# Performance work log

Hardware: AMD Instinct MI355X
Metric: run time of the kernel (lower is better)

Reference implementation:

```python
import jax, jax.numpy as jnp
import numpy as np

BODY_EDGES = [(0, 2), (0, 5), (2, 7), (5, 8), (11, 12), (0, 11), (0, 12), (7, 11), (8, 12), (11, 13), (13, 15), (12, 14), (14, 16), (11, 23), (12, 24), (23, 24), (11, 24), (12, 23)]
N_JOINTS = 33
N_FEAT = 52
HIDDEN = 128
BN_EPS = 1e-5


def _make_adj():
    a = np.eye(N_JOINTS, dtype=np.float32)
    for i, j in BODY_EDGES:
        a[i, j] = 1.0
        a[j, i] = 1.0
    deg = np.clip(a.sum(1), 1.0, None)
    d = deg ** -0.5
    return jnp.asarray(d[:, None] * a * d[None, :])


def setup_inputs() -> dict:
    key = jax.random.key(0)
    ks = iter(jax.random.split(key, 40))
    B, T = 64, 256
    def lin(k, i, o):
        return jax.random.normal(k, (i, o), jnp.float32) / np.sqrt(i)
    inp = {
        'x': jax.random.normal(next(ks), (B, T, N_JOINTS, N_FEAT), jnp.float32),
        'adj': _make_adj(),
        # layer 0: in 52 -> out 128 (has skip linear)
        'W0': lin(next(ks), N_FEAT, HIDDEN), 'b0': jax.random.normal(next(ks), (HIDDEN,)) * 0.02,
        'S0': lin(next(ks), N_FEAT, HIDDEN), 'sb0': jax.random.normal(next(ks), (HIDDEN,)) * 0.02,
        'g0': 1.0 + 0.1 * jax.random.normal(next(ks), (HIDDEN,)), 'be0': 0.1 * jax.random.normal(next(ks), (HIDDEN,)),
        'm0': 0.1 * jax.random.normal(next(ks), (HIDDEN,)), 'v0': 1.0 + 0.1 * jax.random.uniform(next(ks), (HIDDEN,)),
        # layers 1,2: 128 -> 128 (identity skip)
        'W1': lin(next(ks), HIDDEN, HIDDEN), 'b1': jax.random.normal(next(ks), (HIDDEN,)) * 0.02,
        'g1': 1.0 + 0.1 * jax.random.normal(next(ks), (HIDDEN,)), 'be1': 0.1 * jax.random.normal(next(ks), (HIDDEN,)),
        'm1': 0.1 * jax.random.normal(next(ks), (HIDDEN,)), 'v1': 1.0 + 0.1 * jax.random.uniform(next(ks), (HIDDEN,)),
        'W2': lin(next(ks), HIDDEN, HIDDEN), 'b2': jax.random.normal(next(ks), (HIDDEN,)) * 0.02,
        'g2': 1.0 + 0.1 * jax.random.normal(next(ks), (HIDDEN,)), 'be2': 0.1 * jax.random.normal(next(ks), (HIDDEN,)),
        'm2': 0.1 * jax.random.normal(next(ks), (HIDDEN,)), 'v2': 1.0 + 0.1 * jax.random.uniform(next(ks), (HIDDEN,)),
        # temporal attention MLP: 128 -> 128 -> 1
        'tW1': lin(next(ks), HIDDEN, HIDDEN), 'tb1': jax.random.normal(next(ks), (HIDDEN,)) * 0.02,
        'tW2': lin(next(ks), HIDDEN, 1), 'tb2': jax.random.normal(next(ks), (1,)) * 0.02,
    }
    return inp


def _gcn(h, adj, W, b, g, be, m, v, skip):
    # adjacency mix: [B*T, J, D_in]
    a = jnp.einsum('nm,bmd->bnd', adj, h)
    z = a @ W + b
    z = (z - m) * jax.lax.rsqrt(v + BN_EPS) * g + be  # eval-mode BatchNorm1d
    return jax.nn.gelu(z, approximate=False) + skip


def reference(x, adj, W0, b0, S0, sb0, g0, be0, m0, v0,
              W1, b1, g1, be1, m1, v1,
              W2, b2, g2, be2, m2, v2,
              tW1, tb1, tW2, tb2):
    B, T, J, Fd = x.shape
    h = x.reshape(B * T, J, Fd)
    h = _gcn(h, adj, W0, b0, g0, be0, m0, v0, h @ S0 + sb0)
    h = _gcn(h, adj, W1, b1, g1, be1, m1, v1, h)
    h = _gcn(h, adj, W2, b2, g2, be2, m2, v2, h)
    # dropout inactive (eval mode)
    xt = h.mean(axis=1).reshape(B, T, -1)                  # [B, T, H]
    score = jax.nn.gelu(xt @ tW1 + tb1, approximate=False) @ tW2 + tb2  # [B, T, 1]
    attn = jax.nn.softmax(score, axis=1)
    return (xt * attn).sum(axis=1)                         # [B, H]
```

## Files before the change

kernel.cpp:

```cpp
#include <hip/hip_runtime.h>
#include <hip/hip_bf16.h>
#include <math.h>


#define NJ 33
#define NF 52
#define NH 128
#define NT 256
#define NB 64
#define NSAMP (NB*NT)
#define SPB 2
#define NBLKS (NSAMP/SPB)
#define HSTR 136
#define PSTR 40

typedef unsigned short u16;
typedef _Float16 f16;
typedef f16   half8 __attribute__((ext_vector_type(8)));
typedef f16   h2    __attribute__((ext_vector_type(2)));
typedef float f32x4 __attribute__((ext_vector_type(4)));

#define HO_W0    0
#define HO_S0    8192
#define HO_W1    16384
#define HO_W2    32768
#define HO_TW1   49152
#define HO_ADJ32 65536
#define H_TOTAL  66560
#define FO_BASE  (H_TOTAL/2)
#define FO_A0    (FO_BASE+0)
#define FO_SB0   (FO_BASE+768)
#define FO_TB1   (FO_BASE+896)
#define FO_TW2   (FO_BASE+1024)
#define FO_FLG   (FO_BASE+1152)
#define FO_XT    (FO_BASE+1280)
#define FO_SC    (FO_XT + NSAMP*NH)

__device__ __forceinline__ float bf2f(u16 u) { return __uint_as_float(((unsigned)u) << 16); }
__device__ __forceinline__ float ldv(const void* p, long i, int f) {
    float r;
    if (f) r = bf2f(((const u16*)p)[i]);
    else   r = ((const float*)p)[i];
    return r;
}
__device__ int detect_bf16(const void* p) {
    const u16* q = (const u16*)p;
    int nz = 0, ok = 0;
#pragma unroll
    for (int k = 0; k < 64; k++) {
        u16 u = q[k];
        if (u & 0x7FFF) {
            nz++;
            int e = (u >> 7) & 0xFF;
            ok += (e >= 0x40 && e <= 0xBF) ? 1 : 0;
        }
    }
    return (nz == 0) || (ok * 20 >= nz * 19);
}

__device__ __forceinline__ float gelu_c(float x) {
    float xc = fminf(fmaxf(x, -8.f), 8.f);
    float u  = xc * fmaf(xc * xc, 0.10294324f, 2.3022082f);
#if __has_builtin(__builtin_amdgcn_exp2f)
    float e  = __builtin_amdgcn_exp2f(u);
#else
    float e  = exp2f(u);
#endif
#if __has_builtin(__builtin_amdgcn_rcpf)
    float tt = (e - 1.f) * __builtin_amdgcn_rcpf(e + 1.f);
#else
    float tt = (e - 1.f) / (e + 1.f);
#endif
    float hx = 0.5f * x;
    return fmaf(hx, tt, hx);
}

#define MFMA16(a, b, c) __builtin_amdgcn_mfma_f32_16x16x32_f16(a, b, c, 0, 0, 0)

__global__ __launch_bounds__(256) void prep(
    const void* x, const void* adj,
    const void* W0, const void* b0, const void* S0, const void* sb0,
    const void* g0, const void* be0, const void* m0, const void* v0,
    const void* W1, const void* b1, const void* g1, const void* be1, const void* m1, const void* v1,
    const void* W2, const void* b2, const void* g2, const void* be2, const void* m2, const void* v2,
    const void* tW1, const void* tb1, const void* tW2,
    void* ws)
{
    f16* H = (f16*)ws; float* F = (float*)ws;
    const int bi = blockIdx.x, t = threadIdx.x;
    if (bi == 0) {
        const int fW = detect_bf16(W0), fS = detect_bf16(S0);
        for (int i = t; i < NF * 128; i += 256) {
            int k = i >> 7, n = i & 127;
            H[HO_W0 + n * 64 + k] = (f16)ldv(W0, i, fW);
            H[HO_S0 + n * 64 + k] = (f16)ldv(S0, i, fS);
        }
        for (int i = t; i < 128 * 16; i += 256) {
            int n = i >> 4, k = 48 + (i & 15);
            if (k >= NF) { H[HO_W0 + n * 64 + k] = (f16)0.f; H[HO_S0 + n * 64 + k] = (f16)0.f; }
        }
    } else if (bi == 1) {
        const int f = detect_bf16(W1);
        for (int i = t; i < 128 * 128; i += 256) {
            int k = i >> 7, n = i & 127;
            H[HO_W1 + n * 128 + k] = (f16)ldv(W1, i, f);
        }
    } else if (bi == 2) {
        if (t == 0) ((int*)F)[FO_FLG] = detect_bf16(x);
        const int f = detect_bf16(W2);
        for (int i = t; i < 128 * 128; i += 256) {
            int k = i >> 7, n = i & 127;
            H[HO_W2 + n * 128 + k] = (f16)ldv(W2, i, f);
        }
    } else if (bi == 3) {
        const int f = detect_bf16(tW1);
        for (int i = t; i < 128 * 128; i += 256) {
            int k = i >> 7, n = i & 127;
            H[HO_TW1 + n * 128 + k] = (f16)ldv(tW1, i, f);
        }
    } else {
        if (t < 128) {
            int c = t;
            {
                float g = ldv(g0,c,detect_bf16(g0)), be = ldv(be0,c,detect_bf16(be0));
                float m = ldv(m0,c,detect_bf16(m0)), v = ldv(v0,c,detect_bf16(v0));
                float b = ldv(b0,c,detect_bf16(b0));
                float A = g * rsqrtf(v + 1e-5f);
                F[FO_A0 + 0*256 + c] = A; F[FO_A0 + 0*256 + 128 + c] = (b - m)*A + be;
            }
            {
                float g = ldv(g1,c,detect_bf16(g1)), be = ldv(be1,c,detect_bf16(be1));
                float m = ldv(m1,c,detect_bf16(m1)), v = ldv(v1,c,detect_bf16(v1));
                float b = ldv(b1,c,detect_bf16(b1));
                float A = g * rsqrtf(v + 1e-5f);
                F[FO_A0 + 1*256 + c] = A; F[FO_A0 + 1*256 + 128 + c] = (b - m)*A + be;
            }
            {
                float g = ldv(g2,c,detect_bf16(g2)), be = ldv(be2,c,detect_bf16(be2));
                float m = ldv(m2,c,detect_bf16(m2)), v = ldv(v2,c,detect_bf16(v2));
                float b = ldv(b2,c,detect_bf16(b2));
                float A = g * rsqrtf(v + 1e-5f);
                F[FO_A0 + 2*256 + c] = A; F[FO_A0 + 2*256 + 128 + c] = (b - m)*A + be;
            }
            F[FO_SB0 + c] = ldv(sb0, c, detect_bf16(sb0));
            F[FO_TB1 + c] = ldv(tb1, c, detect_bf16(tb1));
            F[FO_TW2 + c] = ldv(tW2, c, detect_bf16(tW2));
        }
        const int fA = detect_bf16(adj);
        for (int i = t; i < 1024; i += 256) {
            int r = i >> 5, c = i & 31;
            float v = (r < 25 && c < 25) ? ldv(adj, (long)r*NJ + c, fA) : 0.f;
            H[HO_ADJ32 + i] = (f16)v;
        }
    }
}

#define PTWRITE(ACC)                                                            \
    _Pragma("unroll")                                                           \
    for (int mt = 0; mt < 4; mt++) {                                            \
        const int fF = mt >> 1;                                                 \
        const int jb = (mt & 1) * 16;                                           \
        _Pragma("unroll")                                                       \
        for (int nt = 0; nt < 2; nt++) {                                        \
            f16* pp = Pt + (fF*128 + (nt ? c1 : c0))*PSTR;                      \
            _Pragma("unroll")                                                   \
            for (int r2 = 0; r2 < 4; r2 += 2) {                                 \
                int j0 = jb + q*4 + r2;                                         \
                if (j0 + 1 < 25) {                                              \
                    h2 v2w = { (f16)ACC[mt][nt][r2], (f16)ACC[mt][nt][r2+1] };  \
                    *(h2*)(pp + j0) = v2w;                                      \
                } else if (j0 < 25) {                                           \
                    pp[j0] = (f16)ACC[mt][nt][r2];                              \
                }                                                               \
            }                                                                   \
        }                                                                       \
    }

#define ADJEPI(L, WRHB) {                                                       \
    f32x4 zac[2][2][2];                                                         \
    _Pragma("unroll")                                                           \
    for (int fF = 0; fF < 2; fF++) {                                            \
        _Pragma("unroll")                                                       \
        for (int nt = 0; nt < 2; nt++) {                                        \
            half8 bz = *(const half8*)(Pt + (fF*128 + (nt?c1:c0))*PSTR + q*8);  \
            zac[fF][0][nt] = MFMA16(afadj0, bz, z4);                            \
            zac[fF][1][nt] = MFMA16(afadj1, bz, z4);                            \
        }                                                                       \
    }                                                                           \
    _Pragma("unroll")                                                           \
    for (int nt = 0; nt < 2; nt++) {                                            \
        const int cc = nt ? c1 : c0;                                            \
        const float Av = rA[L][nt], Dv = rD[L][nt];                             \
        _Pragma("unroll")                                                       \
        for (int fF = 0; fF < 2; fF++) {                                        \
            _Pragma("unroll")                                                   \
            for (int m2 = 0; m2 < 2; m2++) {                                    \
                _Pragma("unroll")                                               \
                for (int r4 = 0; r4 < 4; r4++) {                                \
                    float zv = (m2 == 0) ? zac[fF][0][nt][r4]                   \
                             : (jlt[r4] ? zac[fF][1][nt][r4]                    \
                                        : acc[2*fF+1][nt][r4]);                 \
                    float hnew = gelu_c(fmaf(zv, Av, Dv)) + hz[fF][m2][nt][r4]; \
                    hz[fF][m2][nt][r4] = hnew;                                  \
                    if (WRHB)                                                   \
                        hb[((2*fF+m2)*16 + q*4 + r4)*HSTR + cc] = (f16)hnew;    \
                }                                                               \
            }                                                                   \
            {                                                                   \
                float hnew = gelu_c(fmaf(acc[4][nt][fF], Av, Dv)) + h32[fF][nt];\
                h32[fF][nt] = (q == 0) ? hnew : 0.f;                            \
                if (WRHB && q == 0)                                             \
                    hb[(64 + fF)*HSTR + cc] = (f16)hnew;                        \
            }                                                                   \
        }                                                                       \
    }                                                                           \
}

#define GEMM128(WOFF)                                                           \
    {                                                                           \
        half8 bf[2][4];                                                         \
        _Pragma("unroll")                                                       \
        for (int nt = 0; nt < 2; nt++)                                          \
            _Pragma("unroll")                                                   \
            for (int ks = 0; ks < 4; ks++)                                      \
                bf[nt][ks] = *(const half8*)(HW + (WOFF) + (nt?c1:c0)*128 + ks*32 + q*8); \
        _Pragma("unroll")                                                       \
        for (int mt = 0; mt < 5; mt++) { acc[mt][0] = z4; acc[mt][1] = z4; }    \
        _Pragma("unroll")                                                       \
        for (int mt = 0; mt < 5; mt++) {                                        \
            const int m = mt*16 + ml;                                           \
            _Pragma("unroll")                                                   \
            for (int ks = 0; ks < 4; ks++) {                                    \
                half8 af = *(const half8*)(hb + m*HSTR + ks*32 + q*8);          \
                acc[mt][0] = MFMA16(af, bf[0][ks], acc[mt][0]);                 \
                acc[mt][1] = MFMA16(af, bf[1][ks], acc[mt][1]);                 \
            }                                                                   \
        }                                                                       \
    }

#define GCN_BODY                                                                \
    const f16* HW = (const f16*)ws;                                             \
    float* F = (float*)ws;                                                      \
    float* xt_g = F + FO_XT;                                                    \
    float* sc_g = F + FO_SC;                                                    \
    const int t = threadIdx.x, lane = t & 63, wv = t >> 6;                      \
    const int q = lane >> 4, ml = lane & 15;                                    \
    const int n0 = wv * 32;                                                     \
    const int c0 = n0 + ml, c1 = n0 + 16 + ml;                                  \
    const f32x4 z4 = {0.f, 0.f, 0.f, 0.f};                                      \
    const bool jlt[4] = { q <= 2, q <= 1, q <= 1, q <= 1 };                     \
    const half8 zero8 = {(f16)0.f,(f16)0.f,(f16)0.f,(f16)0.f,(f16)0.f,(f16)0.f,(f16)0.f,(f16)0.f}; \
    _Pragma("unroll")                                                           \
    for (int i = t; i < 512; i += 256) {                                        \
        int fF = i >> 8, rem = i & 255, n = rem >> 1, chh = rem & 1;            \
        *(half8*)(Pt + (fF*128 + n)*PSTR + 24 + chh*8) = zero8;                 \
    }                                                                           \
    float rA[3][2], rD[3][2];                                                   \
    _Pragma("unroll")                                                           \
    for (int L = 0; L < 3; L++) {                                               \
        rA[L][0] = F[FO_A0 + L*256 + c0];        rA[L][1] = F[FO_A0 + L*256 + c1];       \
        rD[L][0] = F[FO_A0 + L*256 + 128 + c0];  rD[L][1] = F[FO_A0 + L*256 + 128 + c1]; \
    }                                                                           \
    const float sb0a = F[FO_SB0 + c0], sb0b = F[FO_SB0 + c1];                   \
    half8 afadj0 = *(const half8*)(HW + HO_ADJ32 + ml*32 + q*8);                \
    half8 afadj1 = *(const half8*)(HW + HO_ADJ32 + (16+ml)*32 + q*8);           \
    __syncthreads();                                                            \
    {                                                                           \
        const int fX = ((const int*)F)[FO_FLG];                                 \
        const long xb = (long)blockIdx.x * (SPB * NJ * NF);                     \
        _Pragma("unroll 1")                                                     \
        for (int it = 0; it < 3; it++) {                                        \
            int g = t + it * 256;                                               \
            if (g < 66 * 8) {                                                   \
                int r = g >> 3, blk = g & 7;                                    \
                int fF = (r >= 33) ? 1 : 0;                                     \
                int j = r - 33 * fF;                                            \
                int fr = (j < 32) ? (fF * 32 + j) : (64 + fF);                  \
                half8 o;                                                        \
                if (!fX) {                                                      \
                    const float* base = (const float*)x + xb + (long)r * NF + blk * 8; \
                    if (blk < 6) {                                              \
                        float4 v0 = *(const float4*)base;                       \
                        float4 v1 = *(const float4*)(base + 4);                 \
                        o[0]=(f16)v0.x; o[1]=(f16)v0.y; o[2]=(f16)v0.z; o[3]=(f16)v0.w; \
                        o[4]=(f16)v1.x; o[5]=(f16)v1.y; o[6]=(f16)v1.z; o[7]=(f16)v1.w; \
                    } else if (blk == 6) {                                      \
                        float4 v0 = *(const float4*)base;                       \
                        o = zero8;                                              \
                        o[0]=(f16)v0.x; o[1]=(f16)v0.y; o[2]=(f16)v0.z; o[3]=(f16)v0.w; \
                    } else o = zero8;                                           \
                } else {                                                        \
                    long rb = xb + (long)r * NF;                                \
                    _Pragma("unroll")                                           \
                    for (int i = 0; i < 8; i++) {                               \
                        int cx = blk * 8 + i;                                   \
                        o[i] = (f16)(cx < NF ? bf2f(((const u16*)x)[rb + cx]) : 0.f); \
                    }                                                           \
                }                                                               \
                *(half8*)(hb + fr * HSTR + blk * 8) = o;                        \
            }                                                                   \
        }                                                                       \
    }                                                                           \
    __syncthreads();                                                            \
    f32x4 acc[5][2];                                                            \
    float hz[2][2][2][4];                                                       \
    float h32[2][2];                                                            \
    {                                                                           \
        half8 bw[2][2], bs[2][2];                                               \
        _Pragma("unroll")                                                       \
        for (int nt = 0; nt < 2; nt++) {                                        \
            int n = nt ? c1 : c0;                                               \
            _Pragma("unroll")                                                   \
            for (int ks = 0; ks < 2; ks++) {                                    \
                bw[nt][ks] = *(const half8*)(HW + HO_W0 + n*64 + ks*32 + q*8);  \
                bs[nt][ks] = *(const half8*)(HW + HO_S0 + n*64 + ks*32 + q*8);  \
            }                                                                   \
        }                                                                       \
        f32x4 acs[5][2];                                                        \
        _Pragma("unroll")                                                       \
        for (int mt = 0; mt < 5; mt++) { acc[mt][0]=z4; acc[mt][1]=z4; acs[mt][0]=z4; acs[mt][1]=z4; } \
        _Pragma("unroll")                                                       \
        for (int mt = 0; mt < 5; mt++) {                                        \
            const int m = mt*16 + ml;                                           \
            half8 a0 = *(const half8*)(hb + m*HSTR + q*8);                      \
            half8 a1 = *(const half8*)(hb + m*HSTR + 32 + q*8);                 \
            acc[mt][0] = MFMA16(a0, bw[0][0], acc[mt][0]);                      \
            acc[mt][0] = MFMA16(a1, bw[0][1], acc[mt][0]);                      \
            acc[mt][1] = MFMA16(a0, bw[1][0], acc[mt][1]);                      \
            acc[mt][1] = MFMA16(a1, bw[1][1], acc[mt][1]);                      \
            acs[mt][0] = MFMA16(a0, bs[0][0], acs[mt][0]);                      \
            acs[mt][0] = MFMA16(a1, bs[0][1], acs[mt][0]);                      \
            acs[mt][1] = MFMA16(a0, bs[1][0], acs[mt][1]);                      \
            acs[mt][1] = MFMA16(a1, bs[1][1], acs[mt][1]);                      \
        }                                                                       \
        __syncthreads();                                                        \
        PTWRITE(acc)                                                            \
        _Pragma("unroll")                                                       \
        for (int fF = 0; fF < 2; fF++)                                          \
            _Pragma("unroll")                                                   \
            for (int m2 = 0; m2 < 2; m2++)                                      \
                _Pragma("unroll")                                               \
                for (int nt = 0; nt < 2; nt++)                                  \
                    _Pragma("unroll")                                           \
                    for (int r4 = 0; r4 < 4; r4++)                              \
                        hz[fF][m2][nt][r4] = acs[2*fF+m2][nt][r4] + (nt ? sb0b : sb0a); \
        _Pragma("unroll")                                                       \
        for (int fF = 0; fF < 2; fF++)                                          \
            _Pragma("unroll")                                                   \
            for (int nt = 0; nt < 2; nt++)                                      \
                h32[fF][nt] = (q == 0) ? (acs[4][nt][fF] + (nt ? sb0b : sb0a)) : 0.f; \
        ADJEPI(0, 1)                                                            \
        __syncthreads();                                                        \
    }                                                                           \
    GEMM128(HO_W1)                                                              \
    __syncthreads();                                                            \
    PTWRITE(acc)                                                                \
    ADJEPI(1, 1)                                                                \
    __syncthreads();                                                            \
    GEMM128(HO_W2)                                                              \
    __syncthreads();                                                            \
    PTWRITE(acc)                                                                \
    ADJEPI(2, 0)                                                                \
    __syncthreads();                                                            \
    _Pragma("unroll")                                                           \
    for (int fF = 0; fF < 2; fF++)                                              \
        _Pragma("unroll")                                                       \
        for (int nt = 0; nt < 2; nt++) {                                        \
            float s = h32[fF][nt];                                              \
            _Pragma("unroll")                                                   \
            for (int m2 = 0; m2 < 2; m2++)                                      \
                _Pragma("unroll")                                               \
                for (int r4 = 0; r4 < 4; r4++) s += hz[fF][m2][nt][r4];         \
            s += __shfl_xor(s, 16, 64);                                         \
            s += __shfl_xor(s, 32, 64);                                         \
            float xtc = s * (1.0f / 33.0f);                                     \
            if (q == 0) {                                                       \
                int cc = nt ? c1 : c0;                                          \
                xtb[fF * 128 + cc] = xtc;                                       \
                xt_g[((long)blockIdx.x * SPB + fF) * NH + cc] = xtc;            \
            }                                                                   \
        }                                                                       \
    __syncthreads();                                                            \
    {                                                                           \
        const int fF = t >> 7, c = t & 127;                                     \
        float u = 0.f;                                                          \
        _Pragma("unroll")                                                       \
        for (int kk = 0; kk < 16; kk++) {                                       \
            half8 wv8 = *(const half8*)(HW + HO_TW1 + c*128 + kk*8);            \
            _Pragma("unroll")                                                   \
            for (int i = 0; i < 8; i++)                                         \
                u = fmaf(xtb[fF*128 + kk*8 + i], (float)wv8[i], u);             \
        }                                                                       \
        float r = gelu_c(u + F[FO_TB1 + c]) * F[FO_TW2 + c];                    \
        _Pragma("unroll")                                                       \
        for (int off = 32; off > 0; off >>= 1) r += __shfl_xor(r, off, 64);     \
        if (lane == 0) rbuf4[wv] = r;                                           \
        __syncthreads();                                                        \
        if (t == 0) {                                                           \
            sc_g[blockIdx.x * SPB + 0] = rbuf4[0] + rbuf4[1];                   \
            sc_g[blockIdx.x * SPB + 1] = rbuf4[2] + rbuf4[3];                   \
        }                                                                       \
    }

__global__ __launch_bounds__(256) void gcn_mfma_a(const void* __restrict__ x,
                                                  void* __restrict__ ws)
{
    __shared__ __align__(16) f16 hb[80 * HSTR];
    __shared__ __align__(16) f16 Pt[2 * 128 * PSTR];
    __shared__ float rbuf4[4];
    float* xtb = (float*)Pt;
    GCN_BODY
}

__global__ __launch_bounds__(256) void gcn_mfma_h(const void* __restrict__ x,
                                                  void* __restrict__ ws)
{
    __shared__ __align__(16) f16 hb[73 * HSTR];
    __shared__ __align__(16) f16 Pt[2 * 128 * PSTR];
    __shared__ float rbuf4[4];
    float* xtb = (float*)Pt;
    GCN_BODY
}

__global__ __launch_bounds__(256) void attn_pool(
    const int* __restrict__ flg,
    const float* __restrict__ xt_ws, const float* __restrict__ score_ws,
    void* __restrict__ out)
{
    __shared__ float ew[NT];
    __shared__ float red[8];
    __shared__ float pb[256];
    const int t = threadIdx.x, lane = t & 63, wv = t >> 6;
    const int b = blockIdx.x >> 2, qr = blockIdx.x & 3;

    float sv = score_ws[b * NT + t];
    float m = sv;
#pragma unroll
    for (int off = 32; off > 0; off >>= 1) m = fmaxf(m, __shfl_xor(m, off, 64));
    if (lane == 0) red[wv] = m;
    __syncthreads();
    float mx = fmaxf(fmaxf(red[0], red[1]), fmaxf(red[2], red[3]));
    float e = __expf(sv - mx);
    ew[t] = e;
    float d = e;
#pragma unroll
    for (int off = 32; off > 0; off >>= 1) d += __shfl_xor(d, off, 64);
    if (lane == 0) red[4 + wv] = d;
    __syncthreads();
    float den = red[4] + red[5] + red[6] + red[7];

    const int cl = t & 31, ch = t >> 5;
    const int c = qr * 32 + cl;
    float a = 0.f;
#pragma unroll 4
    for (int i = ch * 32; i < ch * 32 + 32; i++)
        a = fmaf(ew[i], xt_ws[((long)b * NT + i) * NH + c], a);
    pb[t] = a;
    __syncthreads();
    if (t < 128) pb[t] += pb[t + 128];
    __syncthreads();
    if (t < 64) pb[t] += pb[t + 64];
    __syncthreads();
    if (t < 32) {
        float r = (pb[t] + pb[t + 32]) / den;
        if (*flg) ((__hip_bfloat16*)out)[b * NH + qr * 32 + t] = __float2bfloat16(r);
        else      ((float*)out)[b * NH + qr * 32 + t] = r;
    }
}

extern "C" void kernel_launch(void* const* d_in, const int* in_sizes, int n_in,
                              void* d_out, int out_size, void* d_ws, size_t ws_size,
                              hipStream_t stream) {
    static int use_h = -1;
    if (use_h < 0) {
        hipFuncAttributes a{};
        use_h = 0;
        if (hipFuncGetAttributes(&a, reinterpret_cast<const void*>(gcn_mfma_h)) == hipSuccess
            && a.numRegs > 0 && a.numRegs <= 128
            && a.localSizeBytes == 0)
            use_h = 1;
    }
    prep<<<5, 256, 0, stream>>>(
        d_in[0], d_in[1],
        d_in[2], d_in[3], d_in[4], d_in[5],
        d_in[6], d_in[7], d_in[8], d_in[9],
        d_in[10], d_in[11], d_in[12], d_in[13], d_in[14], d_in[15],
        d_in[16], d_in[17], d_in[18], d_in[19], d_in[20], d_in[21],
        d_in[22], d_in[23], d_in[24],
        d_ws);
    if (use_h) gcn_mfma_h<<<NBLKS, 256, 0, stream>>>(d_in[0], d_ws);
    else       gcn_mfma_a<<<NBLKS, 256, 0, stream>>>(d_in[0], d_ws);
    float* F = (float*)d_ws;
    attn_pool<<<NB * 4, 256, 0, stream>>>((const int*)(F + FO_FLG), F + FO_XT, F + FO_SC, d_out);
}
```

Baseline: 532.3 us.

## Widen GCN kernel to 512 threads with one column tile per wave

The main GCN kernel moves from 256 to 512 threads per block. Each wave now owns 16 output channels instead of 32, which halves the per-thread accumulators and weight fragments so more waves can hide latency. The prep kernel is also parallelised into 65 blocks that transpose the weights through shared-memory tiles, giving coalesced global writes. The trade-off is more waves per block competing for the same shared memory, redundant A-fragment loads across twice as many waves, and a tighter register threshold (64) for choosing the smaller-LDS variant.

```diff
diff --git a/kernel.cpp b/kernel.cpp
--- a/kernel.cpp
+++ b/kernel.cpp
@@ -88,37 +88,32 @@
 {
     f16* H = (f16*)ws; float* F = (float*)ws;
     const int bi = blockIdx.x, t = threadIdx.x;
-    if (bi == 0) {
-        const int fW = detect_bf16(W0), fS = detect_bf16(S0);
-        for (int i = t; i < NF * 128; i += 256) {
-            int k = i >> 7, n = i & 127;
-            H[HO_W0 + n * 64 + k] = (f16)ldv(W0, i, fW);
-            H[HO_S0 + n * 64 + k] = (f16)ldv(S0, i, fS);
+
+    if (bi < 64) {
+        const void* src; int dst, kt, nt, Kvalid, Kd;
+        if (bi < 16)      { src = W1;  dst = HO_W1;  kt = (bi>>2)&3;    nt = bi&3;      Kvalid = 128; Kd = 128; }
+        else if (bi < 32) { src = W2;  dst = HO_W2;  kt = ((bi-16)>>2); nt = (bi-16)&3; Kvalid = 128; Kd = 128; }
+        else if (bi < 48) { src = tW1; dst = HO_TW1; kt = ((bi-32)>>2); nt = (bi-32)&3; Kvalid = 128; Kd = 128; }
+        else if (bi < 56) { src = W0;  dst = HO_W0;  kt = ((bi-48)>>2); nt = (bi-48)&3; Kvalid = NF;  Kd = 64;  }
+        else              { src = S0;  dst = HO_S0;  kt = ((bi-56)>>2); nt = (bi-56)&3; Kvalid = NF;  Kd = 64;  }
+        const int flag = detect_bf16(src);
+        __shared__ float tile[32][33];
+        const int tx = t & 31, ty = t >> 5;
+#pragma unroll
+        for (int r = 0; r < 4; r++) {
+            int k = kt*32 + ty + r*8;
+            int n = nt*32 + tx;
+            tile[ty + r*8][tx] = (k < Kvalid) ? ldv(src, (long)k*128 + n, flag) : 0.f;
         }
-        for (int i = t; i < 128 * 16; i += 256) {
-            int n = i >> 4, k = 48 + (i & 15);
-            if (k >= NF) { H[HO_W0 + n * 64 + k] = (f16)0.f; H[HO_S0 + n * 64 + k] = (f16)0.f; }
-        }
-    } else if (bi == 1) {
-        const int f = detect_bf16(W1);
-        for (int i = t; i < 128 * 128; i += 256) {
-            int k = i >> 7, n = i & 127;
-            H[HO_W1 + n * 128 + k] = (f16)ldv(W1, i, f);
-        }
-    } else if (bi == 2) {
-        if (t == 0) ((int*)F)[FO_FLG] = detect_bf16(x);
-        const int f = detect_bf16(W2);
-        for (int i = t; i < 128 * 128; i += 256) {
-            int k = i >> 7, n = i & 127;
-            H[HO_W2 + n * 128 + k] = (f16)ldv(W2, i, f);
-        }
-    } else if (bi == 3) {
-        const int f = detect_bf16(tW1);
-        for (int i = t; i < 128 * 128; i += 256) {
-            int k = i >> 7, n = i & 127;
-            H[HO_TW1 + n * 128 + k] = (f16)ldv(tW1, i, f);
+        __syncthreads();
+#pragma unroll
+        for (int r = 0; r < 4; r++) {
+            int n = nt*32 + ty + r*8;
+            int k = kt*32 + tx;
+            H[dst + n*Kd + k] = (f16)tile[tx][ty + r*8];
         }
     } else {
+        if (t == 0) ((int*)F)[FO_FLG] = detect_bf16(x);
         if (t < 128) {
             int c = t;
             {
@@ -155,113 +150,98 @@
     }
 }
 
-#define PTWRITE(ACC)                                                            \
+#define ADJEPI_W(L, WRHB) {                                                     \
+    f32x4 zac[2][2];                                                            \
+    _Pragma("unroll")                                                           \
+    for (int fF = 0; fF < 2; fF++) {                                            \
+        half8 bz = *(const half8*)(Pt + (fF*128 + c)*PSTR + q*8);               \
+        zac[fF][0] = MFMA16(afadj0, bz, z4);                                    \
+        zac[fF][1] = MFMA16(afadj1, bz, z4);                                    \
+    }                                                                           \
+    const float Av = rA[L], Dv = rD[L];                                         \
+    _Pragma("unroll")                                                           \
+    for (int fF = 0; fF < 2; fF++) {                                            \
+        _Pragma("unroll")                                                       \
+        for (int m2 = 0; m2 < 2; m2++) {                                        \
+            _Pragma("unroll")                                                   \
+            for (int r4 = 0; r4 < 4; r4++) {                                    \
+                float zv = (m2 == 0) ? zac[fF][0][r4]                           \
+                         : (jlt[r4] ? zac[fF][1][r4] : acc[2*fF+1][r4]);        \
+                float hnew = gelu_c(fmaf(zv, Av, Dv)) + hz[fF][m2][r4];         \
+                hz[fF][m2][r4] = hnew;                                          \
+                if (WRHB)                                                       \
+                    hb[((2*fF+m2)*16 + q*4 + r4)*HSTR + c] = (f16)hnew;         \
+            }                                                                   \
+        }                                                                       \
+        {                                                                       \
+            float hnew = gelu_c(fmaf(acc[4][fF], Av, Dv)) + h32[fF];            \
+            h32[fF] = (q == 0) ? hnew : 0.f;                                    \
+            if (WRHB && q == 0)                                                 \
+                hb[(64 + fF)*HSTR + c] = (f16)hnew;                             \
+        }                                                                       \
+    }                                                                           \
+}
+
+#define PTWRITE_W(ACC)                                                          \
     _Pragma("unroll")                                                           \
     for (int mt = 0; mt < 4; mt++) {                                            \
         const int fF = mt >> 1;                                                 \
         const int jb = (mt & 1) * 16;                                           \
-        _Pragma("unroll")                                                       \
-        for (int nt = 0; nt < 2; nt++) {                                        \
-            f16* pp = Pt + (fF*128 + (nt ? c1 : c0))*PSTR;                      \
-            _Pragma("unroll")                                                   \
-            for (int r2 = 0; r2 < 4; r2 += 2) {                                 \
-                int j0 = jb + q*4 + r2;                                         \
-                if (j0 + 1 < 25) {                                              \
-                    h2 v2w = { (f16)ACC[mt][nt][r2], (f16)ACC[mt][nt][r2+1] };  \
-                    *(h2*)(pp + j0) = v2w;                                      \
-                } else if (j0 < 25) {                                           \
-                    pp[j0] = (f16)ACC[mt][nt][r2];                              \
-                }                                                               \
+        f16* pp = Pt + (fF*128 + c)*PSTR;                                       \
+        _Pragma("unroll")                                                       \
+        for (int r2 = 0; r2 < 4; r2 += 2) {                                     \
+            int j0 = jb + q*4 + r2;                                             \
+            if (j0 + 1 < 25) {                                                  \
+                h2 v2w = { (f16)ACC[mt][r2], (f16)ACC[mt][r2+1] };              \
+                *(h2*)(pp + j0) = v2w;                                          \
+            } else if (j0 < 25) {                                               \
+                pp[j0] = (f16)ACC[mt][r2];                                      \
             }                                                                   \
         }                                                                       \
     }
 
-#define ADJEPI(L, WRHB) {                                                       \
-    f32x4 zac[2][2][2];                                                         \
-    _Pragma("unroll")                                                           \
-    for (int fF = 0; fF < 2; fF++) {                                            \
-        _Pragma("unroll")                                                       \
-        for (int nt = 0; nt < 2; nt++) {                                        \
-            half8 bz = *(const half8*)(Pt + (fF*128 + (nt?c1:c0))*PSTR + q*8);  \
-            zac[fF][0][nt] = MFMA16(afadj0, bz, z4);                            \
-            zac[fF][1][nt] = MFMA16(afadj1, bz, z4);                            \
-        }                                                                       \
-    }                                                                           \
-    _Pragma("unroll")                                                           \
-    for (int nt = 0; nt < 2; nt++) {                                            \
-        const int cc = nt ? c1 : c0;                                            \
-        const float Av = rA[L][nt], Dv = rD[L][nt];                             \
-        _Pragma("unroll")                                                       \
-        for (int fF = 0; fF < 2; fF++) {                                        \
-            _Pragma("unroll")                                                   \
-            for (int m2 = 0; m2 < 2; m2++) {                                    \
-                _Pragma("unroll")                                               \
-                for (int r4 = 0; r4 < 4; r4++) {                                \
-                    float zv = (m2 == 0) ? zac[fF][0][nt][r4]                   \
-                             : (jlt[r4] ? zac[fF][1][nt][r4]                    \
-                                        : acc[2*fF+1][nt][r4]);                 \
-                    float hnew = gelu_c(fmaf(zv, Av, Dv)) + hz[fF][m2][nt][r4]; \
-                    hz[fF][m2][nt][r4] = hnew;                                  \
-                    if (WRHB)                                                   \
-                        hb[((2*fF+m2)*16 + q*4 + r4)*HSTR + cc] = (f16)hnew;    \
-                }                                                               \
-            }                                                                   \
-            {                                                                   \
-                float hnew = gelu_c(fmaf(acc[4][nt][fF], Av, Dv)) + h32[fF][nt];\
-                h32[fF][nt] = (q == 0) ? hnew : 0.f;                            \
-                if (WRHB && q == 0)                                             \
-                    hb[(64 + fF)*HSTR + cc] = (f16)hnew;                        \
-            }                                                                   \
-        }                                                                       \
-    }                                                                           \
-}
-
-#define GEMM128(WOFF)                                                           \
+#define GEMM128_W(WOFF)                                                         \
     {                                                                           \
-        half8 bf[2][4];                                                         \
-        _Pragma("unroll")                                                       \
-        for (int nt = 0; nt < 2; nt++)                                          \
-            _Pragma("unroll")                                                   \
-            for (int ks = 0; ks < 4; ks++)                                      \
-                bf[nt][ks] = *(const half8*)(HW + (WOFF) + (nt?c1:c0)*128 + ks*32 + q*8); \
-        _Pragma("unroll")                                                       \
-        for (int mt = 0; mt < 5; mt++) { acc[mt][0] = z4; acc[mt][1] = z4; }    \
+        half8 bf[4];                                                            \
+        _Pragma("unroll")                                                       \
+        for (int ks = 0; ks < 4; ks++)                                          \
+            bf[ks] = *(const half8*)(HW + (WOFF) + c*128 + ks*32 + q*8);        \
+        _Pragma("unroll")                                                       \
+        for (int mt = 0; mt < 5; mt++) acc[mt] = z4;                            \
         _Pragma("unroll")                                                       \
         for (int mt = 0; mt < 5; mt++) {                                        \
             const int m = mt*16 + ml;                                           \
             _Pragma("unroll")                                                   \
             for (int ks = 0; ks < 4; ks++) {                                    \
                 half8 af = *(const half8*)(hb + m*HSTR + ks*32 + q*8);          \
-                acc[mt][0] = MFMA16(af, bf[0][ks], acc[mt][0]);                 \
-                acc[mt][1] = MFMA16(af, bf[1][ks], acc[mt][1]);                 \
+                acc[mt] = MFMA16(af, bf[ks], acc[mt]);                          \
             }                                                                   \
         }                                                                       \
     }
 
-#define GCN_BODY                                                                \
+#define GCN_W_BODY                                                              \
+    float* xtb = (float*)Pt;                                                    \
     const f16* HW = (const f16*)ws;                                             \
     float* F = (float*)ws;                                                      \
     float* xt_g = F + FO_XT;                                                    \
     float* sc_g = F + FO_SC;                                                    \
     const int t = threadIdx.x, lane = t & 63, wv = t >> 6;                      \
     const int q = lane >> 4, ml = lane & 15;                                    \
-    const int n0 = wv * 32;                                                     \
-    const int c0 = n0 + ml, c1 = n0 + 16 + ml;                                  \
+    const int c = wv * 16 + ml;                                                 \
     const f32x4 z4 = {0.f, 0.f, 0.f, 0.f};                                      \
     const bool jlt[4] = { q <= 2, q <= 1, q <= 1, q <= 1 };                     \
     const half8 zero8 = {(f16)0.f,(f16)0.f,(f16)0.f,(f16)0.f,(f16)0.f,(f16)0.f,(f16)0.f,(f16)0.f}; \
-    _Pragma("unroll")                                                           \
-    for (int i = t; i < 512; i += 256) {                                        \
-        int fF = i >> 8, rem = i & 255, n = rem >> 1, chh = rem & 1;            \
+    {                                                                           \
+        int fF = t >> 8, rem = t & 255, n = rem >> 1, chh = rem & 1;            \
         *(half8*)(Pt + (fF*128 + n)*PSTR + 24 + chh*8) = zero8;                 \
     }                                                                           \
-    float rA[3][2], rD[3][2];                                                   \
+    float rA[3], rD[3];                                                         \
     _Pragma("unroll")                                                           \
     for (int L = 0; L < 3; L++) {                                               \
-        rA[L][0] = F[FO_A0 + L*256 + c0];        rA[L][1] = F[FO_A0 + L*256 + c1];       \
-        rD[L][0] = F[FO_A0 + L*256 + 128 + c0];  rD[L][1] = F[FO_A0 + L*256 + 128 + c1]; \
-    }                                                                           \
-    const float sb0a = F[FO_SB0 + c0], sb0b = F[FO_SB0 + c1];                   \
+        rA[L] = F[FO_A0 + L*256 + c];                                           \
+        rD[L] = F[FO_A0 + L*256 + 128 + c];                                     \
+    }                                                                           \
+    const float sb0v = F[FO_SB0 + c];                                           \
     half8 afadj0 = *(const half8*)(HW + HO_ADJ32 + ml*32 + q*8);                \
     half8 afadj1 = *(const half8*)(HW + HO_ADJ32 + (16+ml)*32 + q*8);           \
     __syncthreads();                                                            \
@@ -269,8 +249,8 @@
         const int fX = ((const int*)F)[FO_FLG];                                 \
         const long xb = (long)blockIdx.x * (SPB * NJ * NF);                     \
         _Pragma("unroll 1")                                                     \
-        for (int it = 0; it < 3; it++) {                                        \
-            int g = t + it * 256;                                               \
+        for (int it = 0; it < 2; it++) {                                        \
+            int g = t + it * 512;                                               \
             if (g < 66 * 8) {                                                   \
                 int r = g >> 3, blk = g & 7;                                    \
                 int fF = (r >= 33) ? 1 : 0;                                     \
@@ -302,99 +282,87 @@
         }                                                                       \
     }                                                                           \
     __syncthreads();                                                            \
-    f32x4 acc[5][2];                                                            \
-    float hz[2][2][2][4];                                                       \
-    float h32[2][2];                                                            \
+    f32x4 acc[5];                                                               \
+    float hz[2][2][4];                                                          \
+    float h32[2];                                                               \
     {                                                                           \
-        half8 bw[2][2], bs[2][2];                                               \
-        _Pragma("unroll")                                                       \
-        for (int nt = 0; nt < 2; nt++) {                                        \
-            int n = nt ? c1 : c0;                                               \
-            _Pragma("unroll")                                                   \
-            for (int ks = 0; ks < 2; ks++) {                                    \
-                bw[nt][ks] = *(const half8*)(HW + HO_W0 + n*64 + ks*32 + q*8);  \
-                bs[nt][ks] = *(const half8*)(HW + HO_S0 + n*64 + ks*32 + q*8);  \
-            }                                                                   \
-        }                                                                       \
-        f32x4 acs[5][2];                                                        \
-        _Pragma("unroll")                                                       \
-        for (int mt = 0; mt < 5; mt++) { acc[mt][0]=z4; acc[mt][1]=z4; acs[mt][0]=z4; acs[mt][1]=z4; } \
+        half8 bw[2], bs[2];                                                     \
+        _Pragma("unroll")                                                       \
+        for (int ks = 0; ks < 2; ks++) {                                        \
+            bw[ks] = *(const half8*)(HW + HO_W0 + c*64 + ks*32 + q*8);          \
+            bs[ks] = *(const half8*)(HW + HO_S0 + c*64 + ks*32 + q*8);          \
+        }                                                                       \
+        f32x4 acs[5];                                                           \
+        _Pragma("unroll")                                                       \
+        for (int mt = 0; mt < 5; mt++) { acc[mt] = z4; acs[mt] = z4; }          \
         _Pragma("unroll")                                                       \
         for (int mt = 0; mt < 5; mt++) {                                        \
             const int m = mt*16 + ml;                                           \
             half8 a0 = *(const half8*)(hb + m*HSTR + q*8);                      \
             half8 a1 = *(const half8*)(hb + m*HSTR + 32 + q*8);                 \
-            acc[mt][0] = MFMA16(a0, bw[0][0], acc[mt][0]);                      \
-            acc[mt][0] = MFMA16(a1, bw[0][1], acc[mt][0]);                      \
-            acc[mt][1] = MFMA16(a0, bw[1][0], acc[mt][1]);                      \
-            acc[mt][1] = MFMA16(a1, bw[1][1], acc[mt][1]);                      \
-            acs[mt][0] = MFMA16(a0, bs[0][0], acs[mt][0]);                      \
-            acs[mt][0] = MFMA16(a1, bs[0][1], acs[mt][0]);                      \
-            acs[mt][1] = MFMA16(a0, bs[1][0], acs[mt][1]);                      \
-            acs[mt][1] = MFMA16(a1, bs[1][1], acs[mt][1]);                      \
+            acc[mt] = MFMA16(a0, bw[0], acc[mt]);                               \
+            acc[mt] = MFMA16(a1, bw[1], acc[mt]);                               \
+            acs[mt] = MFMA16(a0, bs[0], acs[mt]);                               \
+            acs[mt] = MFMA16(a1, bs[1], acs[mt]);                               \
         }                                                                       \
         __syncthreads();                                                        \
-        PTWRITE(acc)                                                            \
+        PTWRITE_W(acc)                                                          \
         _Pragma("unroll")                                                       \
         for (int fF = 0; fF < 2; fF++)                                          \
             _Pragma("unroll")                                                   \
             for (int m2 = 0; m2 < 2; m2++)                                      \
                 _Pragma("unroll")                                               \
-                for (int nt = 0; nt < 2; nt++)                                  \
-                    _Pragma("unroll")                                           \
-                    for (int r4 = 0; r4 < 4; r4++)                              \
-                        hz[fF][m2][nt][r4] = acs[2*fF+m2][nt][r4] + (nt ? sb0b : sb0a); \
+                for (int r4 = 0; r4 < 4; r4++)                                  \
+                    hz[fF][m2][r4] = acs[2*fF+m2][r4] + sb0v;                   \
         _Pragma("unroll")                                                       \
         for (int fF = 0; fF < 2; fF++)                                          \
+            h32[fF] = (q == 0) ? (acs[4][fF] + sb0v) : 0.f;                     \
+    }                                                                           \
+    ADJEPI_W(0, 1)                                                              \
+    __syncthreads();                                                            \
+    GEMM128_W(HO_W1)                                                            \
+    __syncthreads();                                                            \
+    PTWRITE_W(acc)                                                              \
+    ADJEPI_W(1, 1)                                                              \
+    __syncthreads();                                                            \
+    GEMM128_W(HO_W2)                                                            \
+    __syncthreads();                                                            \
+    PTWRITE_W(acc)                                                              \
+    ADJEPI_W(2, 0)                                                              \
+    __syncthreads();                                                            \
+    _Pragma("unroll")                                                           \
+    for (int fF = 0; fF < 2; fF++) {                                            \
+        float s = h32[fF];                                                      \
+        _Pragma("unroll")                                                       \
+        for (int m2 = 0; m2 < 2; m2++)                                          \
             _Pragma("unroll")                                                   \
-            for (int nt = 0; nt < 2; nt++)                                      \
-                h32[fF][nt] = (q == 0) ? (acs[4][nt][fF] + (nt ? sb0b : sb0a)) : 0.f; \
-        ADJEPI(0, 1)                                                            \
-        __syncthreads();                                                        \
-    }                                                                           \
-    GEMM128(HO_W1)                                                              \
-    __syncthreads();                                                            \
-    PTWRITE(acc)                                                                \
-    ADJEPI(1, 1)                                                                \
-    __syncthreads();                                                            \
-    GEMM128(HO_W2)                                                              \
-    __syncthreads();                                                            \
-    PTWRITE(acc)                                                                \
-    ADJEPI(2, 0)                                                                \
-    __syncthreads();                                                            \
-    _Pragma("unroll")                                                           \
-    for (int fF = 0; fF < 2; fF++)                                              \
-        _Pragma("unroll")                                                       \
-        for (int nt = 0; nt < 2; nt++) {                                        \
-            float s = h32[fF][nt];                                              \
+            for (int r4 = 0; r4 < 4; r4++) s += hz[fF][m2][r4];                 \
+        s += __shfl_xor(s, 16, 64);                                             \
+        s += __shfl_xor(s, 32, 64);                                             \
+        float xtc = s * (1.0f / 33.0f);                                         \
+        if (q == 0) {                                                           \
+            xtb[fF * 128 + c] = xtc;                                            \
+            xt_g[((long)blockIdx.x * SPB + fF) * NH + c] = xtc;                 \
+        }                                                                       \
+    }                                                                           \
+    __syncthreads();                                                            \
+    {                                                                           \
+        float r = 0.f;                                                          \
+        if (t < 256) {                                                          \
+            const int fF = t >> 7, ch = t & 127;                                \
+            float u = 0.f;                                                      \
             _Pragma("unroll")                                                   \
-            for (int m2 = 0; m2 < 2; m2++)                                      \
+            for (int kk = 0; kk < 16; kk++) {                                   \
+                half8 wv8 = *(const half8*)(HW + HO_TW1 + ch*128 + kk*8);       \
                 _Pragma("unroll")                                               \
-                for (int r4 = 0; r4 < 4; r4++) s += hz[fF][m2][nt][r4];         \
-            s += __shfl_xor(s, 16, 64);                                         \
-            s += __shfl_xor(s, 32, 64);                                         \
-            float xtc = s * (1.0f / 33.0f);                                     \
-            if (q == 0) {                                                       \
-                int cc = nt ? c1 : c0;                                          \
-                xtb[fF * 128 + cc] = xtc;                                       \
-                xt_g[((long)blockIdx.x * SPB + fF) * NH + cc] = xtc;            \
+                for (int i = 0; i < 8; i++)                                     \
+                    u = fmaf(xtb[fF*128 + kk*8 + i], (float)wv8[i], u);         \
             }                                                                   \
-        }                                                                       \
-    __syncthreads();                                                            \
-    {                                                                           \
-        const int fF = t >> 7, c = t & 127;                                     \
-        float u = 0.f;                                                          \
-        _Pragma("unroll")                                                       \
-        for (int kk = 0; kk < 16; kk++) {                                       \
-            half8 wv8 = *(const half8*)(HW + HO_TW1 + c*128 + kk*8);            \
-            _Pragma("unroll")                                                   \
-            for (int i = 0; i < 8; i++)                                         \
-                u = fmaf(xtb[fF*128 + kk*8 + i], (float)wv8[i], u);             \
-        }                                                                       \
-        float r = gelu_c(u + F[FO_TB1 + c]) * F[FO_TW2 + c];                    \
+            r = gelu_c(u + F[FO_TB1 + ch]) * F[FO_TW2 + ch];                    \
+        }                                                                       \
         _Pragma("unroll")                                                       \
         for (int off = 32; off > 0; off >>= 1) r += __shfl_xor(r, off, 64);     \
-        if (lane == 0) rbuf4[wv] = r;                                           \
+        if (lane == 0 && wv < 4) rbuf4[wv] = r;                                 \
         __syncthreads();                                                        \
         if (t == 0) {                                                           \
             sc_g[blockIdx.x * SPB + 0] = rbuf4[0] + rbuf4[1];                   \
@@ -402,24 +370,22 @@
         }                                                                       \
     }
 
-__global__ __launch_bounds__(256) void gcn_mfma_a(const void* __restrict__ x,
+__global__ __launch_bounds__(512) void gcn_mfma_w(const void* __restrict__ x,
                                                   void* __restrict__ ws)
 {
     __shared__ __align__(16) f16 hb[80 * HSTR];
     __shared__ __align__(16) f16 Pt[2 * 128 * PSTR];
     __shared__ float rbuf4[4];
-    float* xtb = (float*)Pt;
-    GCN_BODY
-}
-
-__global__ __launch_bounds__(256) void gcn_mfma_h(const void* __restrict__ x,
-                                                  void* __restrict__ ws)
+    GCN_W_BODY
+}
+
+__global__ __launch_bounds__(512) void gcn_mfma_w73(const void* __restrict__ x,
+                                                    void* __restrict__ ws)
 {
     __shared__ __align__(16) f16 hb[73 * HSTR];
     __shared__ __align__(16) f16 Pt[2 * 128 * PSTR];
     __shared__ float rbuf4[4];
-    float* xtb = (float*)Pt;
-    GCN_BODY
+    GCN_W_BODY
 }
 
 __global__ __launch_bounds__(256) void attn_pool(
@@ -471,16 +437,16 @@
 extern "C" void kernel_launch(void* const* d_in, const int* in_sizes, int n_in,
                               void* d_out, int out_size, void* d_ws, size_t ws_size,
                               hipStream_t stream) {
-    static int use_h = -1;
-    if (use_h < 0) {
+    static int use_73 = -1;
+    if (use_73 < 0) {
         hipFuncAttributes a{};
-        use_h = 0;
-        if (hipFuncGetAttributes(&a, reinterpret_cast<const void*>(gcn_mfma_h)) == hipSuccess
-            && a.numRegs > 0 && a.numRegs <= 128
+        use_73 = 0;
+        if (hipFuncGetAttributes(&a, reinterpret_cast<const void*>(gcn_mfma_w73)) == hipSuccess
+            && a.numRegs > 0 && a.numRegs <= 64
             && a.localSizeBytes == 0)
-            use_h = 1;
-    }
-    prep<<<5, 256, 0, stream>>>(
+            use_73 = 1;
+    }
+    prep<<<65, 256, 0, stream>>>(
         d_in[0], d_in[1],
         d_in[2], d_in[3], d_in[4], d_in[5],
         d_in[6], d_in[7], d_in[8], d_in[9],
@@ -488,8 +454,8 @@
         d_in[16], d_in[17], d_in[18], d_in[19], d_in[20], d_in[21],
         d_in[22], d_in[23], d_in[24],
         d_ws);
-    if (use_h) gcn_mfma_h<<<NBLKS, 256, 0, stream>>>(d_in[0], d_ws);
-    else       gcn_mfma_a<<<NBLKS, 256, 0, stream>>>(d_in[0], d_ws);
+    if (use_73) gcn_mfma_w73<<<NBLKS, 512, 0, stream>>>(d_in[0], d_ws);
+    else        gcn_mfma_w<<<NBLKS, 512, 0, stream>>>(d_in[0], d_ws);
     float* F = (float*)d_ws;
     attn_pool<<<NB * 4, 256, 0, stream>>>((const int*)(F + FO_FLG), F + FO_XT, F + FO_SC, d_out);
 }
```

New measurement: 505.3 us. 1.05x faster.
